# Kernel tuning notes

Hardware: AMD Instinct MI355X
Metric: run time of the kernel (lower is better)

Reference implementation:

```python
import jax, jax.numpy as jnp
import numpy as np

# PM-field / module constants (from module source + plausible PMField defaults)
DT = 0.1          # PM-field integration step
EPS = 1e-4        # softening of gravitational flow
PM_STEPS = 4      # pm_steps
TAU = 0.9         # membrane_tau
M_GAIN = 0.1      # membrane_gain
EI_GAIN = 0.06    # VectorizedLateralEI gain
PLR = 0.001       # plasticity_lr (mu_lr = c_lr)


def setup_inputs() -> dict:
    key = jax.random.key(0)
    ks = jax.random.split(key, 8)
    B, D_IN, D_HID, D_LAT, N_C, CH, N_CLS = 16384, 784, 256, 8, 64, 64, 10
    x = jax.random.normal(ks[0], (B, D_IN), jnp.float32)
    W1 = jax.random.normal(ks[1], (D_IN, D_HID), jnp.float32) * 0.05
    b1 = jnp.zeros((D_HID,), jnp.float32)
    W2 = jax.random.normal(ks[2], (D_HID, D_LAT), jnp.float32) * 0.05
    b2 = jnp.zeros((D_LAT,), jnp.float32)
    mu = jax.random.uniform(ks[3], (N_C,), jnp.float32) * 0.5       # center strengths
    c = jax.random.normal(ks[4], (N_C, D_LAT), jnp.float32)         # center positions
    Wp = jax.random.normal(ks[5], (D_LAT, CH), jnp.float32) * 0.3
    bp = jnp.zeros((CH,), jnp.float32)
    Wr = jax.random.normal(ks[6], (CH, N_CLS), jnp.float32) * 0.1
    br = jnp.zeros((N_CLS,), jnp.float32)
    return {"x": x, "W1": W1, "b1": b1, "W2": W2, "b2": b2, "mu": mu,
            "c": c, "Wp": Wp, "bp": bp, "Wr": Wr, "br": br, "T": 5}


def _pm_evolve(z, mu, c):
    # Gravitational PM-field: z follows softened attraction to centers c with strengths mu.
    def body(z, _):
        d = c[None, :, :] - z[:, None, :]            # [B, N, D]
        r2 = jnp.sum(d * d, axis=-1) + EPS           # [B, N]
        z = z + DT * jnp.einsum('bn,bnd->bd', mu / r2, d)
        return z, None
    z, _ = jax.lax.scan(body, z, None, length=PM_STEPS)
    return z


def _forward(x, W1, b1, W2, b2, mu, c, Wp, bp, Wr, br, T):
    z = jnp.tanh(x @ W1 + b1) @ W2 + b2              # enc: [B, d_latent]
    h = jnp.zeros((x.shape[0], Wp.shape[1]), x.dtype)

    def step(carry, _):
        z, h, mu, c = carry
        z_ev = _pm_evolve(z, mu, c)
        h_proj = jnp.tanh(z_ev @ Wp + bp)
        h_new = TAU * h + M_GAIN * h_proj
        # lateral EI: excitation minus mean inhibition
        h_f = h_new + EI_GAIN * (h_new - jnp.mean(h_new, axis=-1, keepdims=True))
        logits = h_f @ Wr + br
        # vectorized Hebbian plasticity on PM centers (no-grad, like torch .data update)
        d = c[None, :, :] - z_ev[:, None, :]
        r2 = jnp.sum(d * d, axis=-1)                 # [B, N]
        act = jnp.exp(-r2)                           # center activity
        post = jnp.mean(h_f, axis=-1)                # postsynaptic drive [B]
        mu2 = mu + PLR * jnp.mean(act * post[:, None], axis=0)
        wsum = jnp.sum(act, axis=0)                  # [N]
        w = act / (wsum + EPS)[None, :]
        c2 = c + PLR * (jnp.einsum('bn,bd->nd', w, z_ev) - c * (wsum / (wsum + EPS))[:, None])
        mu2 = jax.lax.stop_gradient(mu2)
        c2 = jax.lax.stop_gradient(c2)
        return (z_ev, h_f, mu2, c2), logits

    (z, h, _, _), logits_seq = jax.lax.scan(step, (z, h, mu, c), None, length=T)
    return logits_seq[-1], z, h


def reference(x, W1, b1, W2, b2, mu, c, Wp, bp, Wr, br, T):
    return _forward(x, W1, b1, W2, b2, mu, c, Wp, bp, Wr, br, T)
```

## Files before the change

### kernel.cpp

```cpp
#include <hip/hip_runtime.h>
#include <math.h>

#define B_N     16384
#define D_IN    784
#define D_HID   256
#define D_LAT   8
#define N_CTR   64
#define CH_N    64
#define N_CLS   10

#define DT_C    0.1f
#define EPS_C   1e-4f
#define PM_STEPS 4
#define TAU_C   0.9f
#define MGAIN   0.1f
#define EIG     0.06f
#define PLR_C   0.001f
#define T_STEPS 5

#define KP      832

typedef short bf16x8 __attribute__((ext_vector_type(8)));
typedef float f32x4v __attribute__((ext_vector_type(4)));

__device__ __forceinline__ void split_pair(float a, float b, unsigned& hi, unsigned& lo) {
    unsigned ua = __float_as_uint(a), ub = __float_as_uint(b);
    hi = (ua >> 16) | (ub & 0xffff0000u);
    float ra = a - __uint_as_float(ua & 0xffff0000u);
    float rb = b - __uint_as_float(ub & 0xffff0000u);
    lo = (__float_as_uint(ra) >> 16) | (__float_as_uint(rb) & 0xffff0000u);
}

__device__ __forceinline__ float fast_rcp(float x) { return __builtin_amdgcn_rcpf(x); }
__device__ __forceinline__ float fast_tanh(float a) {
    float e = __expf(2.0f * a);
    return 1.0f - 2.0f * fast_rcp(e + 1.0f);
}

#define DPP_XOR_ADD(v, CTRL) \
    ((v) + __int_as_float(__builtin_amdgcn_update_dpp(0, __float_as_int(v), (CTRL), 0xF, 0xF, true)))

__global__ __launch_bounds__(256) void w1t_kernel(
    const float* __restrict__ W1, ushort* __restrict__ WtH, ushort* __restrict__ WtL)
{
    __shared__ float t[32][36];
    const int kb = blockIdx.x;
    const int nb = blockIdx.y;
    const int tid = threadIdx.x;
    {
        const int r = tid >> 3, c4 = (tid & 7) * 4;
        const int k = kb * 32 + r;
        float4 v = {0.f, 0.f, 0.f, 0.f};
        if (k < D_IN) v = *(const float4*)(W1 + (size_t)k * 256 + nb * 32 + c4);
        t[r][c4 + 0] = v.x; t[r][c4 + 1] = v.y; t[r][c4 + 2] = v.z; t[r][c4 + 3] = v.w;
    }
    __syncthreads();
    const int n = tid >> 3, kq = (tid & 7) * 4;
    float a0 = t[kq + 0][n], a1 = t[kq + 1][n], a2 = t[kq + 2][n], a3 = t[kq + 3][n];
    unsigned h0, l0, h1w, l1w;
    split_pair(a0, a1, h0, l0);
    split_pair(a2, a3, h1w, l1w);
    const size_t o = (size_t)(nb * 32 + n) * KP + kb * 32 + kq;
    uint2 hv; hv.x = h0; hv.y = h1w;
    uint2 lv; lv.x = l0; lv.y = l1w;
    *(uint2*)(WtH + o) = hv;
    *(uint2*)(WtL + o) = lv;
}

__global__ __launch_bounds__(256, 3) void enc1_kernel(
    const float* __restrict__ x, const ushort* __restrict__ WtH,
    const ushort* __restrict__ WtL, const float* __restrict__ b1,
    float* __restrict__ h1)
{
    __shared__ alignas(16) unsigned char AhiS[16384];
    __shared__ alignas(16) unsigned char AloS[16384];
    __shared__ alignas(16) unsigned char BhiS[8192];
    __shared__ alignas(16) unsigned char BloS[8192];

    const int tid = threadIdx.x;
    const int bx  = blockIdx.x;
    const int wk  = (bx & 7) * 64 + (bx >> 3);
    const int n0  = (wk & 3) * 64;
    const int m0  = (wk >> 2) * 128;

    const int m_s = tid >> 1, kh = tid & 1;
    const int n_s = tid >> 2, kq = tid & 3;
    const float*  xrow = x + (size_t)(m0 + m_s) * D_IN;
    const ushort* bhrow = WtH + (size_t)(n0 + n_s) * KP + kq * 16;
    const ushort* blrow = WtL + (size_t)(n0 + n_s) * KP + kq * 16;
    const unsigned offB0 = (unsigned)(n_s * 128) + (unsigned)(((2 * kq)     ^ (n_s & 7)) << 4);
    const unsigned offB1 = (unsigned)(n_s * 128) + (unsigned)(((2 * kq + 1) ^ (n_s & 7)) << 4);

    const int lane = tid & 63;
    const int wid  = tid >> 6;
    const int wm   = wid >> 1, wn = wid & 1;
    const int fr   = lane & 15, g = lane >> 4;
    const unsigned swz = (unsigned)((fr & 7) << 4);
    const int kgb  = g * 16;

    f32x4v acc[4][2];
    #pragma unroll
    for (int mi = 0; mi < 4; ++mi)
        #pragma unroll
        for (int ni = 0; ni < 2; ++ni) acc[mi][ni] = (f32x4v){0.f, 0.f, 0.f, 0.f};

    for (int kt = 0; kt < 13; ++kt) {
        const int kbase = kt * 64 + kh * 32;
        float4 av[8];
        #pragma unroll
        for (int q = 0; q < 8; ++q) {
            const int kk = kbase + q * 4;
            float4 z4 = {0.f, 0.f, 0.f, 0.f};
            av[q] = (kk < D_IN) ? *(const float4*)(xrow + kk) : z4;
        }
        #pragma unroll
        for (int q16 = 0; q16 < 4; ++q16) {
            uint4 hw, lw;
            split_pair(av[2 * q16].x,     av[2 * q16].y,     hw.x, lw.x);
            split_pair(av[2 * q16].z,     av[2 * q16].w,     hw.y, lw.y);
            split_pair(av[2 * q16 + 1].x, av[2 * q16 + 1].y, hw.z, lw.z);
            split_pair(av[2 * q16 + 1].z, av[2 * q16 + 1].w, hw.w, lw.w);
            const unsigned off = (unsigned)(m_s * 128) +
                (unsigned)((((kh * 4 + q16) ^ (m_s & 7))) << 4);
            *(uint4*)(AhiS + off) = hw;
            *(uint4*)(AloS + off) = lw;
        }
        {
            const int ko = kt * 64;
            uint4 h0 = *(const uint4*)(bhrow + ko);
            uint4 h1v = *(const uint4*)(bhrow + ko + 8);
            uint4 l0 = *(const uint4*)(blrow + ko);
            uint4 l1v = *(const uint4*)(blrow + ko + 8);
            *(uint4*)(BhiS + offB0) = h0;
            *(uint4*)(BhiS + offB1) = h1v;
            *(uint4*)(BloS + offB0) = l0;
            *(uint4*)(BloS + offB1) = l1v;
        }
        __syncthreads();

        #pragma unroll
        for (int ks = 0; ks < 2; ++ks) {
            const unsigned kb = (unsigned)(ks * 64 + kgb);
            bf16x8 ahv[4], alv[4];
            #pragma unroll
            for (int mi = 0; mi < 4; ++mi) {
                const unsigned off = (unsigned)((wm * 64 + mi * 16 + fr) * 128) + (kb ^ swz);
                ahv[mi] = *(const bf16x8*)(AhiS + off);
                alv[mi] = *(const bf16x8*)(AloS + off);
            }
            #pragma unroll
            for (int ni = 0; ni < 2; ++ni) {
                const unsigned offb = (unsigned)((wn * 32 + ni * 16 + fr) * 128) + (kb ^ swz);
                bf16x8 bh = *(const bf16x8*)(BhiS + offb);
                bf16x8 bl = *(const bf16x8*)(BloS + offb);
                #pragma unroll
                for (int mi = 0; mi < 4; ++mi) {
                    acc[mi][ni] = __builtin_amdgcn_mfma_f32_16x16x32_bf16(ahv[mi], bh, acc[mi][ni], 0, 0, 0);
                    acc[mi][ni] = __builtin_amdgcn_mfma_f32_16x16x32_bf16(ahv[mi], bl, acc[mi][ni], 0, 0, 0);
                    acc[mi][ni] = __builtin_amdgcn_mfma_f32_16x16x32_bf16(alv[mi], bh, acc[mi][ni], 0, 0, 0);
                }
            }
        }
        __syncthreads();
    }

    #pragma unroll
    for (int ni = 0; ni < 2; ++ni) {
        const int col = n0 + wn * 32 + ni * 16 + fr;
        const float bias = b1[col];
        #pragma unroll
        for (int mi = 0; mi < 4; ++mi) {
            #pragma unroll
            for (int r = 0; r < 4; ++r) {
                const int row = m0 + wm * 64 + mi * 16 + g * 4 + r;
                h1[(size_t)row * 256 + col] = tanhf(acc[mi][ni][r] + bias);
            }
        }
    }
}

__global__ __launch_bounds__(256) void enc2_kernel(
    const float* __restrict__ h1, const float* __restrict__ W2,
    const float* __restrict__ b2, float* __restrict__ zT)
{
    __shared__ alignas(16) float hs[32][260];
    __shared__ alignas(16) float w2t[8][260];
    const int tid = threadIdx.x;
    const int r0 = blockIdx.x * 32;
    for (int i = tid; i < D_HID * D_LAT; i += 256) {
        int k = i >> 3, d = i & 7;
        w2t[d][k] = W2[i];
    }
    #pragma unroll
    for (int i = 0; i < 8; ++i) {
        int idx = tid + i * 256;
        int rr = idx >> 6, c4 = idx & 63;
        float4 v = *(const float4*)(h1 + (size_t)(r0 + rr) * D_HID + c4 * 4);
        *(float4*)&hs[rr][c4 * 4] = v;
    }
    __syncthreads();
    const int r = tid >> 3, d = tid & 7;
    float acc = 0.f;
    #pragma unroll 8
    for (int k4 = 0; k4 < 64; ++k4) {
        float4 a = *(const float4*)&hs[r][k4 * 4];
        float4 w = *(const float4*)&w2t[d][k4 * 4];
        acc = fmaf(a.x, w.x, acc);
        acc = fmaf(a.y, w.y, acc);
        acc = fmaf(a.z, w.z, acc);
        acc = fmaf(a.w, w.w, acc);
    }
    zT[(size_t)(r0 + r) * 8 + d] = acc + b2[d];
}

__global__ __launch_bounds__(256) void stepA2_kernel(
    float* __restrict__ zT, float* __restrict__ hT,
    const float* __restrict__ mu, const float* __restrict__ c,
    const float* __restrict__ Wp, const float* __restrict__ bp,
    const float* __restrict__ Wr, const float* __restrict__ br,
    float* __restrict__ part, float* __restrict__ out, int t)
{
    __shared__ alignas(16) float mu_s[64];
    __shared__ alignas(16) float c_s[512];
    __shared__ alignas(16) float wp_s[512];
    __shared__ alignas(16) float bp_s[64];
    __shared__ alignas(16) float wr_s[704];
    __shared__ alignas(16) float br_s[16];
    __shared__ alignas(16) float act_s[32 * 72];
    __shared__ alignas(16) float z_s[256];
    __shared__ alignas(16) float post_s[32];
    __shared__ alignas(16) float red2[4 * 64 * 10];
    const int tid = threadIdx.x;
    if (tid < 64) { mu_s[tid] = mu[tid]; bp_s[tid] = bp[tid]; }
    for (int i = tid; i < 512; i += 256) { c_s[i] = c[i]; wp_s[i] = Wp[i]; }
    const bool last = (t == T_STEPS - 1);
    if (last) {
        for (int i = tid; i < 640; i += 256) wr_s[(i / 10) * 11 + (i % 10)] = Wr[i];
        if (tid < N_CLS) br_s[tid] = br[tid];
    }
    __syncthreads();

    const int sub  = tid & 7;
    const int grp  = tid >> 3;
    const int b    = blockIdx.x * 32 + grp;
    const int lane = tid & 63;
    const int gbase = lane & ~7;

    float zown = zT[(size_t)b * 8 + sub];
    float z[8];
    #pragma unroll
    for (int d = 0; d < 8; ++d) z[d] = __shfl(zown, gbase + d, 64);

    #pragma unroll 1
    for (int it = 0; it < PM_STEPS; ++it) {
        float f[8];
        #pragma unroll
        for (int d = 0; d < 8; ++d) f[d] = 0.f;
        #pragma unroll
        for (int k = 0; k < 8; ++k) {
            const int n = sub + 8 * k;
            float dx[8];
            float r2 = EPS_C;
            #pragma unroll
            for (int d = 0; d < 8; ++d) {
                dx[d] = c_s[n * 8 + d] - z[d];
                r2 = fmaf(dx[d], dx[d], r2);
            }
            float wgt = mu_s[n] * fast_rcp(r2);
            #pragma unroll
            for (int d = 0; d < 8; ++d) f[d] = fmaf(wgt, dx[d], f[d]);
        }
        #pragma unroll
        for (int d = 0; d < 8; ++d) f[d] = DPP_XOR_ADD(f[d], 0xB1);
        #pragma unroll
        for (int d = 0; d < 8; ++d) f[d] = DPP_XOR_ADD(f[d], 0x4E);
        #pragma unroll
        for (int d = 0; d < 8; ++d) f[d] += __shfl_xor(f[d], 4, 64);
        #pragma unroll
        for (int d = 0; d < 8; ++d) z[d] = fmaf(DT_C, f[d], z[d]);
    }
    float zsel = z[0];
    #pragma unroll
    for (int d = 1; d < 8; ++d) if (sub == d) zsel = z[d];
    zT[(size_t)b * 8 + sub] = zsel;

    float hn[8];
    float s = 0.f;
    #pragma unroll
    for (int j = 0; j < 8; ++j) {
        const int ch = sub * 8 + j;
        float a = bp_s[ch];
        #pragma unroll
        for (int d = 0; d < 8; ++d) a = fmaf(z[d], wp_s[d * 64 + ch], a);
        hn[j] = fast_tanh(a);
    }
    if (t == 0) {
        #pragma unroll
        for (int j = 0; j < 8; ++j) { hn[j] = MGAIN * hn[j]; s += hn[j]; }
    } else {
        const float4* hp = (const float4*)(hT + (size_t)b * 64 + sub * 8);
        float4 h0 = hp[0], h1v = hp[1];
        hn[0] = TAU_C * h0.x + MGAIN * hn[0];
        hn[1] = TAU_C * h0.y + MGAIN * hn[1];
        hn[2] = TAU_C * h0.z + MGAIN * hn[2];
        hn[3] = TAU_C * h0.w + MGAIN * hn[3];
        hn[4] = TAU_C * h1v.x + MGAIN * hn[4];
        hn[5] = TAU_C * h1v.y + MGAIN * hn[5];
        hn[6] = TAU_C * h1v.z + MGAIN * hn[6];
        hn[7] = TAU_C * h1v.w + MGAIN * hn[7];
        #pragma unroll
        for (int j = 0; j < 8; ++j) s += hn[j];
    }
    s = DPP_XOR_ADD(s, 0xB1);
    s = DPP_XOR_ADD(s, 0x4E);
    s += __shfl_xor(s, 4, 64);
    const float mean = s * (1.f / 64.f);
    float spost = 0.f;
    #pragma unroll
    for (int j = 0; j < 8; ++j) {
        hn[j] = hn[j] + EIG * (hn[j] - mean);
        spost += hn[j];
    }
    {
        float4 a0 = {hn[0], hn[1], hn[2], hn[3]};
        float4 a1 = {hn[4], hn[5], hn[6], hn[7]};
        float4* hp = (float4*)(hT + (size_t)b * 64 + sub * 8);
        hp[0] = a0; hp[1] = a1;
    }
    spost = DPP_XOR_ADD(spost, 0xB1);
    spost = DPP_XOR_ADD(spost, 0x4E);
    spost += __shfl_xor(spost, 4, 64);

    if (!last) {
        z_s[tid] = zsel;
        if (sub == 0) post_s[grp] = spost * (1.f / 64.f);
        #pragma unroll
        for (int k = 0; k < 8; ++k) {
            const int n = sub + 8 * k;
            float r2 = 0.f;
            #pragma unroll
            for (int d = 0; d < 8; ++d) {
                float dd = c_s[n * 8 + d] - z[d];
                r2 = fmaf(dd, dd, r2);
            }
            act_s[grp * 72 + n] = __expf(-r2);
        }
        __syncthreads();
        const int q = tid >> 6, n2 = tid & 63;
        float r[10];
        #pragma unroll
        for (int j = 0; j < 10; ++j) r[j] = 0.f;
        #pragma unroll
        for (int i = 0; i < 8; ++i) {
            const int g2 = q * 8 + i;
            float a = act_s[g2 * 72 + n2];
            const float4* zp = (const float4*)&z_s[g2 * 8];
            float4 za = zp[0], zb = zp[1];
            r[0] += a;
            r[1] = fmaf(a, post_s[g2], r[1]);
            r[2] = fmaf(a, za.x, r[2]);
            r[3] = fmaf(a, za.y, r[3]);
            r[4] = fmaf(a, za.z, r[4]);
            r[5] = fmaf(a, za.w, r[5]);
            r[6] = fmaf(a, zb.x, r[6]);
            r[7] = fmaf(a, zb.y, r[7]);
            r[8] = fmaf(a, zb.z, r[8]);
            r[9] = fmaf(a, zb.w, r[9]);
        }
        #pragma unroll
        for (int j = 0; j < 10; ++j) red2[(q * 64 + n2) * 10 + j] = r[j];
        __syncthreads();
        if (q == 0) {
            #pragma unroll
            for (int j = 0; j < 10; ++j) {
                float sv = (red2[(n2) * 10 + j] + red2[(64 + n2) * 10 + j]) +
                           (red2[(128 + n2) * 10 + j] + red2[(192 + n2) * 10 + j]);
                part[((size_t)blockIdx.x * 64 + n2) * 10 + j] = sv;
            }
        }
    } else {
        float lg[N_CLS];
        #pragma unroll
        for (int cls = 0; cls < N_CLS; ++cls) lg[cls] = 0.f;
        #pragma unroll
        for (int j = 0; j < 8; ++j) {
            const int ch = sub * 8 + j;
            #pragma unroll
            for (int cls = 0; cls < N_CLS; ++cls)
                lg[cls] = fmaf(hn[j], wr_s[ch * 11 + cls], lg[cls]);
        }
        #pragma unroll
        for (int cls = 0; cls < N_CLS; ++cls) {
            lg[cls] = DPP_XOR_ADD(lg[cls], 0xB1);
            lg[cls] = DPP_XOR_ADD(lg[cls], 0x4E);
            lg[cls] += __shfl_xor(lg[cls], 4, 64);
        }
        if (sub == 0) {
            #pragma unroll
            for (int cls = 0; cls < N_CLS; ++cls)
                out[(size_t)b * 10 + cls] = lg[cls] + br_s[cls];
        }
        out[163840 + (size_t)b * 8 + sub] = zsel;
        {
            float4 a0 = {hn[0], hn[1], hn[2], hn[3]};
            float4 a1 = {hn[4], hn[5], hn[6], hn[7]};
            float4* op = (float4*)(out + 294912 + (size_t)b * 64 + sub * 8);
            op[0] = a0; op[1] = a1;
        }
    }
}

__global__ __launch_bounds__(256) void stepB2_kernel(
    const float* __restrict__ part,
    const float* __restrict__ mu_in, const float* __restrict__ c_in,
    float* __restrict__ mu_out, float* __restrict__ c_out)
{
    const int n = blockIdx.x, tid = threadIdx.x;
    __shared__ float red[256][10];
    const float* p0 = part + ((size_t)tid * 64 + n) * 10;
    const float* p1 = part + ((size_t)(tid + 256) * 64 + n) * 10;
    #pragma unroll
    for (int j = 0; j < 10; ++j) red[tid][j] = p0[j] + p1[j];
    __syncthreads();
    for (int s = 128; s > 0; s >>= 1) {
        if (tid < s) {
            #pragma unroll
            for (int j = 0; j < 10; ++j) red[tid][j] += red[tid + s][j];
        }
        __syncthreads();
    }
    if (tid == 0) {
        const float S1 = red[0][0];
        const float S2 = red[0][1] * (1.f / B_N);
        mu_out[n] = mu_in[n] + PLR_C * S2;
        const float denom = S1 + EPS_C;
        #pragma unroll
        for (int d = 0; d < 8; ++d) {
            float s3 = red[0][2 + d];
            c_out[n * 8 + d] = c_in[n * 8 + d] + PLR_C * (s3 / denom - c_in[n * 8 + d] * (S1 / denom));
        }
    }
}

extern "C" void kernel_launch(void* const* d_in, const int* in_sizes, int n_in,
                              void* d_out, int out_size, void* d_ws, size_t ws_size,
                              hipStream_t stream) {
    (void)in_sizes; (void)n_in; (void)out_size; (void)ws_size;
    const float* x   = (const float*)d_in[0];
    const float* W1  = (const float*)d_in[1];
    const float* b1  = (const float*)d_in[2];
    const float* W2  = (const float*)d_in[3];
    const float* b2  = (const float*)d_in[4];
    const float* mu0 = (const float*)d_in[5];
    const float* c0  = (const float*)d_in[6];
    const float* Wp  = (const float*)d_in[7];
    const float* bp  = (const float*)d_in[8];
    const float* Wr  = (const float*)d_in[9];
    const float* br  = (const float*)d_in[10];
    float* out = (float*)d_out;
    float* ws  = (float*)d_ws;

    float* h1    = ws;
    float* hT    = ws;
    float* part  = ws + 2113536;
    float* zT    = ws + 4194304;
    float* mu_buf = ws + 4325376;
    float* c_buf  = ws + 4325504;
    ushort* WtH  = (ushort*)(ws + 4326528);
    ushort* WtL  = (ushort*)(ws + 4433024);

    w1t_kernel<<<dim3(26, 8), 256, 0, stream>>>(W1, WtH, WtL);
    enc1_kernel<<<512, 256, 0, stream>>>(x, WtH, WtL, b1, h1);
    enc2_kernel<<<512, 256, 0, stream>>>(h1, W2, b2, zT);

    const float* mu_cur = mu0;
    const float* c_cur  = c0;
    for (int t = 0; t < T_STEPS; ++t) {
        stepA2_kernel<<<512, 256, 0, stream>>>(zT, hT, mu_cur, c_cur, Wp, bp, Wr, br,
                                               part, out, t);
        if (t < T_STEPS - 1) {
            float* mo = mu_buf + (t & 1) * 64;
            float* co = c_buf  + (t & 1) * 512;
            stepB2_kernel<<<64, 256, 0, stream>>>(part, mu_cur, c_cur, mo, co);
            mu_cur = mo;
            c_cur  = co;
        }
    }
}
```

Baseline: 120.1 us.

## Halve per-block tiles in encoder GEMM and step kernel to double block count

The enc1 GEMM tile shrinks from 128x64 to 64x64 rows per block, with half the LDS for A, and launch bounds raised to 4 blocks per SIMD with 1024 blocks. stepA2 now uses 16 lanes per sample instead of 8, with 16 samples per block across 1024 blocks, a 16-lane DPP/shuffle reduction macro, and a padded stride-9 centre array in LDS to avoid bank conflicts. stepB2 sums four partial rows per thread to match the doubled partial count. The aim is more parallelism and occupancy on the many-CU GPU, at the cost of less data reuse per block in the GEMM and more partial sums to reduce.

```diff
diff --git a/kernel.cpp b/kernel.cpp
--- a/kernel.cpp
+++ b/kernel.cpp
@@ -37,8 +37,14 @@
     return 1.0f - 2.0f * fast_rcp(e + 1.0f);
 }
 
-#define DPP_XOR_ADD(v, CTRL) \
+#define DPP_ADD(v, CTRL) \
     ((v) + __int_as_float(__builtin_amdgcn_update_dpp(0, __float_as_int(v), (CTRL), 0xF, 0xF, true)))
+#define RED16(v) do { \
+    v = DPP_ADD(v, 0xB1); \
+    v = DPP_ADD(v, 0x4E); \
+    v += __shfl_xor(v, 4, 64); \
+    v = DPP_ADD(v, 0x128); \
+} while (0)
 
 __global__ __launch_bounds__(256) void w1t_kernel(
     const float* __restrict__ W1, ushort* __restrict__ WtH, ushort* __restrict__ WtL)
@@ -67,27 +73,29 @@
     *(uint2*)(WtL + o) = lv;
 }
 
-__global__ __launch_bounds__(256, 3) void enc1_kernel(
+__global__ __launch_bounds__(256, 4) void enc1_kernel(
     const float* __restrict__ x, const ushort* __restrict__ WtH,
     const ushort* __restrict__ WtL, const float* __restrict__ b1,
     float* __restrict__ h1)
 {
-    __shared__ alignas(16) unsigned char AhiS[16384];
-    __shared__ alignas(16) unsigned char AloS[16384];
+    __shared__ alignas(16) unsigned char AhiS[8192];
+    __shared__ alignas(16) unsigned char AloS[8192];
     __shared__ alignas(16) unsigned char BhiS[8192];
     __shared__ alignas(16) unsigned char BloS[8192];
 
     const int tid = threadIdx.x;
     const int bx  = blockIdx.x;
-    const int wk  = (bx & 7) * 64 + (bx >> 3);
+    const int wk  = (bx & 7) * 128 + (bx >> 3);
     const int n0  = (wk & 3) * 64;
-    const int m0  = (wk >> 2) * 128;
-
-    const int m_s = tid >> 1, kh = tid & 1;
+    const int m0  = (wk >> 2) * 64;
+
+    const int m_s = tid >> 2, kq2 = tid & 3;
     const int n_s = tid >> 2, kq = tid & 3;
     const float*  xrow = x + (size_t)(m0 + m_s) * D_IN;
     const ushort* bhrow = WtH + (size_t)(n0 + n_s) * KP + kq * 16;
     const ushort* blrow = WtL + (size_t)(n0 + n_s) * KP + kq * 16;
+    const unsigned offA0 = (unsigned)(m_s * 128) + (unsigned)(((2 * kq2)     ^ (m_s & 7)) << 4);
+    const unsigned offA1 = (unsigned)(m_s * 128) + (unsigned)(((2 * kq2 + 1) ^ (m_s & 7)) << 4);
     const unsigned offB0 = (unsigned)(n_s * 128) + (unsigned)(((2 * kq)     ^ (n_s & 7)) << 4);
     const unsigned offB1 = (unsigned)(n_s * 128) + (unsigned)(((2 * kq + 1) ^ (n_s & 7)) << 4);
 
@@ -98,32 +106,35 @@
     const unsigned swz = (unsigned)((fr & 7) << 4);
     const int kgb  = g * 16;
 
-    f32x4v acc[4][2];
-    #pragma unroll
-    for (int mi = 0; mi < 4; ++mi)
+    f32x4v acc[2][2];
+    #pragma unroll
+    for (int mi = 0; mi < 2; ++mi)
         #pragma unroll
         for (int ni = 0; ni < 2; ++ni) acc[mi][ni] = (f32x4v){0.f, 0.f, 0.f, 0.f};
 
     for (int kt = 0; kt < 13; ++kt) {
-        const int kbase = kt * 64 + kh * 32;
-        float4 av[8];
-        #pragma unroll
-        for (int q = 0; q < 8; ++q) {
-            const int kk = kbase + q * 4;
-            float4 z4 = {0.f, 0.f, 0.f, 0.f};
-            av[q] = (kk < D_IN) ? *(const float4*)(xrow + kk) : z4;
-        }
-        #pragma unroll
-        for (int q16 = 0; q16 < 4; ++q16) {
-            uint4 hw, lw;
-            split_pair(av[2 * q16].x,     av[2 * q16].y,     hw.x, lw.x);
-            split_pair(av[2 * q16].z,     av[2 * q16].w,     hw.y, lw.y);
-            split_pair(av[2 * q16 + 1].x, av[2 * q16 + 1].y, hw.z, lw.z);
-            split_pair(av[2 * q16 + 1].z, av[2 * q16 + 1].w, hw.w, lw.w);
-            const unsigned off = (unsigned)(m_s * 128) +
-                (unsigned)((((kh * 4 + q16) ^ (m_s & 7))) << 4);
-            *(uint4*)(AhiS + off) = hw;
-            *(uint4*)(AloS + off) = lw;
+        {
+            const int kbase = kt * 64 + kq2 * 16;
+            float4 av[4];
+            #pragma unroll
+            for (int q = 0; q < 4; ++q) {
+                const int kk = kbase + q * 4;
+                float4 z4 = {0.f, 0.f, 0.f, 0.f};
+                av[q] = (kk < D_IN) ? *(const float4*)(xrow + kk) : z4;
+            }
+            uint4 hw0, lw0, hw1, lw1;
+            split_pair(av[0].x, av[0].y, hw0.x, lw0.x);
+            split_pair(av[0].z, av[0].w, hw0.y, lw0.y);
+            split_pair(av[1].x, av[1].y, hw0.z, lw0.z);
+            split_pair(av[1].z, av[1].w, hw0.w, lw0.w);
+            split_pair(av[2].x, av[2].y, hw1.x, lw1.x);
+            split_pair(av[2].z, av[2].w, hw1.y, lw1.y);
+            split_pair(av[3].x, av[3].y, hw1.z, lw1.z);
+            split_pair(av[3].z, av[3].w, hw1.w, lw1.w);
+            *(uint4*)(AhiS + offA0) = hw0;
+            *(uint4*)(AhiS + offA1) = hw1;
+            *(uint4*)(AloS + offA0) = lw0;
+            *(uint4*)(AloS + offA1) = lw1;
         }
         {
             const int ko = kt * 64;
@@ -141,10 +152,10 @@
         #pragma unroll
         for (int ks = 0; ks < 2; ++ks) {
             const unsigned kb = (unsigned)(ks * 64 + kgb);
-            bf16x8 ahv[4], alv[4];
-            #pragma unroll
-            for (int mi = 0; mi < 4; ++mi) {
-                const unsigned off = (unsigned)((wm * 64 + mi * 16 + fr) * 128) + (kb ^ swz);
+            bf16x8 ahv[2], alv[2];
+            #pragma unroll
+            for (int mi = 0; mi < 2; ++mi) {
+                const unsigned off = (unsigned)((wm * 32 + mi * 16 + fr) * 128) + (kb ^ swz);
                 ahv[mi] = *(const bf16x8*)(AhiS + off);
                 alv[mi] = *(const bf16x8*)(AloS + off);
             }
@@ -154,7 +165,7 @@
                 bf16x8 bh = *(const bf16x8*)(BhiS + offb);
                 bf16x8 bl = *(const bf16x8*)(BloS + offb);
                 #pragma unroll
-                for (int mi = 0; mi < 4; ++mi) {
+                for (int mi = 0; mi < 2; ++mi) {
                     acc[mi][ni] = __builtin_amdgcn_mfma_f32_16x16x32_bf16(ahv[mi], bh, acc[mi][ni], 0, 0, 0);
                     acc[mi][ni] = __builtin_amdgcn_mfma_f32_16x16x32_bf16(ahv[mi], bl, acc[mi][ni], 0, 0, 0);
                     acc[mi][ni] = __builtin_amdgcn_mfma_f32_16x16x32_bf16(alv[mi], bh, acc[mi][ni], 0, 0, 0);
@@ -169,10 +180,10 @@
         const int col = n0 + wn * 32 + ni * 16 + fr;
         const float bias = b1[col];
         #pragma unroll
-        for (int mi = 0; mi < 4; ++mi) {
+        for (int mi = 0; mi < 2; ++mi) {
             #pragma unroll
             for (int r = 0; r < 4; ++r) {
-                const int row = m0 + wm * 64 + mi * 16 + g * 4 + r;
+                const int row = m0 + wm * 32 + mi * 16 + g * 4 + r;
                 h1[(size_t)row * 256 + col] = tanhf(acc[mi][ni][r] + bias);
             }
         }
@@ -221,18 +232,21 @@
     float* __restrict__ part, float* __restrict__ out, int t)
 {
     __shared__ alignas(16) float mu_s[64];
-    __shared__ alignas(16) float c_s[512];
+    __shared__ alignas(16) float c9_s[576];
     __shared__ alignas(16) float wp_s[512];
     __shared__ alignas(16) float bp_s[64];
     __shared__ alignas(16) float wr_s[704];
     __shared__ alignas(16) float br_s[16];
-    __shared__ alignas(16) float act_s[32 * 72];
-    __shared__ alignas(16) float z_s[256];
-    __shared__ alignas(16) float post_s[32];
+    __shared__ alignas(16) float act_s[16 * 72];
+    __shared__ alignas(16) float z_s[128];
+    __shared__ alignas(16) float post_s[16];
     __shared__ alignas(16) float red2[4 * 64 * 10];
     const int tid = threadIdx.x;
     if (tid < 64) { mu_s[tid] = mu[tid]; bp_s[tid] = bp[tid]; }
-    for (int i = tid; i < 512; i += 256) { c_s[i] = c[i]; wp_s[i] = Wp[i]; }
+    for (int i = tid; i < 512; i += 256) {
+        c9_s[(i >> 3) * 9 + (i & 7)] = c[i];
+        wp_s[i] = Wp[i];
+    }
     const bool last = (t == T_STEPS - 1);
     if (last) {
         for (int i = tid; i < 640; i += 256) wr_s[(i / 10) * 11 + (i % 10)] = Wr[i];
@@ -240,13 +254,13 @@
     }
     __syncthreads();
 
-    const int sub  = tid & 7;
-    const int grp  = tid >> 3;
-    const int b    = blockIdx.x * 32 + grp;
+    const int sub  = tid & 15;
+    const int grp  = tid >> 4;
+    const int b    = blockIdx.x * 16 + grp;
     const int lane = tid & 63;
-    const int gbase = lane & ~7;
-
-    float zown = zT[(size_t)b * 8 + sub];
+    const int gbase = lane & ~15;
+
+    float zown = zT[(size_t)b * 8 + (sub & 7)];
     float z[8];
     #pragma unroll
     for (int d = 0; d < 8; ++d) z[d] = __shfl(zown, gbase + d, 64);
@@ -257,13 +271,13 @@
         #pragma unroll
         for (int d = 0; d < 8; ++d) f[d] = 0.f;
         #pragma unroll
-        for (int k = 0; k < 8; ++k) {
-            const int n = sub + 8 * k;
+        for (int k = 0; k < 4; ++k) {
+            const int n = sub + 16 * k;
             float dx[8];
             float r2 = EPS_C;
             #pragma unroll
             for (int d = 0; d < 8; ++d) {
-                dx[d] = c_s[n * 8 + d] - z[d];
+                dx[d] = c9_s[n * 9 + d] - z[d];
                 r2 = fmaf(dx[d], dx[d], r2);
             }
             float wgt = mu_s[n] * fast_rcp(r2);
@@ -271,24 +285,20 @@
             for (int d = 0; d < 8; ++d) f[d] = fmaf(wgt, dx[d], f[d]);
         }
         #pragma unroll
-        for (int d = 0; d < 8; ++d) f[d] = DPP_XOR_ADD(f[d], 0xB1);
-        #pragma unroll
-        for (int d = 0; d < 8; ++d) f[d] = DPP_XOR_ADD(f[d], 0x4E);
-        #pragma unroll
-        for (int d = 0; d < 8; ++d) f[d] += __shfl_xor(f[d], 4, 64);
+        for (int d = 0; d < 8; ++d) RED16(f[d]);
         #pragma unroll
         for (int d = 0; d < 8; ++d) z[d] = fmaf(DT_C, f[d], z[d]);
     }
     float zsel = z[0];
     #pragma unroll
-    for (int d = 1; d < 8; ++d) if (sub == d) zsel = z[d];
-    zT[(size_t)b * 8 + sub] = zsel;
-
-    float hn[8];
+    for (int d = 1; d < 8; ++d) if ((sub & 7) == d) zsel = z[d];
+    if (sub < 8) zT[(size_t)b * 8 + sub] = zsel;
+
+    float hn[4];
     float s = 0.f;
     #pragma unroll
-    for (int j = 0; j < 8; ++j) {
-        const int ch = sub * 8 + j;
+    for (int j = 0; j < 4; ++j) {
+        const int ch = sub * 4 + j;
         float a = bp_s[ch];
         #pragma unroll
         for (int d = 0; d < 8; ++d) a = fmaf(z[d], wp_s[d * 64 + ch], a);
@@ -296,51 +306,40 @@
     }
     if (t == 0) {
         #pragma unroll
-        for (int j = 0; j < 8; ++j) { hn[j] = MGAIN * hn[j]; s += hn[j]; }
+        for (int j = 0; j < 4; ++j) { hn[j] = MGAIN * hn[j]; s += hn[j]; }
     } else {
-        const float4* hp = (const float4*)(hT + (size_t)b * 64 + sub * 8);
-        float4 h0 = hp[0], h1v = hp[1];
+        float4 h0 = *(const float4*)(hT + (size_t)b * 64 + sub * 4);
         hn[0] = TAU_C * h0.x + MGAIN * hn[0];
         hn[1] = TAU_C * h0.y + MGAIN * hn[1];
         hn[2] = TAU_C * h0.z + MGAIN * hn[2];
         hn[3] = TAU_C * h0.w + MGAIN * hn[3];
-        hn[4] = TAU_C * h1v.x + MGAIN * hn[4];
-        hn[5] = TAU_C * h1v.y + MGAIN * hn[5];
-        hn[6] = TAU_C * h1v.z + MGAIN * hn[6];
-        hn[7] = TAU_C * h1v.w + MGAIN * hn[7];
-        #pragma unroll
-        for (int j = 0; j < 8; ++j) s += hn[j];
-    }
-    s = DPP_XOR_ADD(s, 0xB1);
-    s = DPP_XOR_ADD(s, 0x4E);
-    s += __shfl_xor(s, 4, 64);
+        #pragma unroll
+        for (int j = 0; j < 4; ++j) s += hn[j];
+    }
+    RED16(s);
     const float mean = s * (1.f / 64.f);
     float spost = 0.f;
     #pragma unroll
-    for (int j = 0; j < 8; ++j) {
+    for (int j = 0; j < 4; ++j) {
         hn[j] = hn[j] + EIG * (hn[j] - mean);
         spost += hn[j];
     }
     {
         float4 a0 = {hn[0], hn[1], hn[2], hn[3]};
-        float4 a1 = {hn[4], hn[5], hn[6], hn[7]};
-        float4* hp = (float4*)(hT + (size_t)b * 64 + sub * 8);
-        hp[0] = a0; hp[1] = a1;
-    }
-    spost = DPP_XOR_ADD(spost, 0xB1);
-    spost = DPP_XOR_ADD(spost, 0x4E);
-    spost += __shfl_xor(spost, 4, 64);
+        *(float4*)(hT + (size_t)b * 64 + sub * 4) = a0;
+    }
+    RED16(spost);
 
     if (!last) {
-        z_s[tid] = zsel;
+        if (sub < 8) z_s[grp * 8 + sub] = zsel;
         if (sub == 0) post_s[grp] = spost * (1.f / 64.f);
         #pragma unroll
-        for (int k = 0; k < 8; ++k) {
-            const int n = sub + 8 * k;
+        for (int k = 0; k < 4; ++k) {
+            const int n = sub + 16 * k;
             float r2 = 0.f;
             #pragma unroll
             for (int d = 0; d < 8; ++d) {
-                float dd = c_s[n * 8 + d] - z[d];
+                float dd = c9_s[n * 9 + d] - z[d];
                 r2 = fmaf(dd, dd, r2);
             }
             act_s[grp * 72 + n] = __expf(-r2);
@@ -351,8 +350,8 @@
         #pragma unroll
         for (int j = 0; j < 10; ++j) r[j] = 0.f;
         #pragma unroll
-        for (int i = 0; i < 8; ++i) {
-            const int g2 = q * 8 + i;
+        for (int i = 0; i < 4; ++i) {
+            const int g2 = q * 4 + i;
             float a = act_s[g2 * 72 + n2];
             const float4* zp = (const float4*)&z_s[g2 * 8];
             float4 za = zp[0], zb = zp[1];
@@ -383,29 +382,23 @@
         #pragma unroll
         for (int cls = 0; cls < N_CLS; ++cls) lg[cls] = 0.f;
         #pragma unroll
-        for (int j = 0; j < 8; ++j) {
-            const int ch = sub * 8 + j;
+        for (int j = 0; j < 4; ++j) {
+            const int ch = sub * 4 + j;
             #pragma unroll
             for (int cls = 0; cls < N_CLS; ++cls)
                 lg[cls] = fmaf(hn[j], wr_s[ch * 11 + cls], lg[cls]);
         }
         #pragma unroll
-        for (int cls = 0; cls < N_CLS; ++cls) {
-            lg[cls] = DPP_XOR_ADD(lg[cls], 0xB1);
-            lg[cls] = DPP_XOR_ADD(lg[cls], 0x4E);
-            lg[cls] += __shfl_xor(lg[cls], 4, 64);
-        }
+        for (int cls = 0; cls < N_CLS; ++cls) RED16(lg[cls]);
         if (sub == 0) {
             #pragma unroll
             for (int cls = 0; cls < N_CLS; ++cls)
                 out[(size_t)b * 10 + cls] = lg[cls] + br_s[cls];
         }
-        out[163840 + (size_t)b * 8 + sub] = zsel;
+        if (sub < 8) out[163840 + (size_t)b * 8 + sub] = zsel;
         {
             float4 a0 = {hn[0], hn[1], hn[2], hn[3]};
-            float4 a1 = {hn[4], hn[5], hn[6], hn[7]};
-            float4* op = (float4*)(out + 294912 + (size_t)b * 64 + sub * 8);
-            op[0] = a0; op[1] = a1;
+            *(float4*)(out + 294912 + (size_t)b * 64 + sub * 4) = a0;
         }
     }
 }
@@ -417,10 +410,12 @@
 {
     const int n = blockIdx.x, tid = threadIdx.x;
     __shared__ float red[256][10];
-    const float* p0 = part + ((size_t)tid * 64 + n) * 10;
+    const float* p0 = part + ((size_t)(tid)       * 64 + n) * 10;
     const float* p1 = part + ((size_t)(tid + 256) * 64 + n) * 10;
-    #pragma unroll
-    for (int j = 0; j < 10; ++j) red[tid][j] = p0[j] + p1[j];
+    const float* p2 = part + ((size_t)(tid + 512) * 64 + n) * 10;
+    const float* p3 = part + ((size_t)(tid + 768) * 64 + n) * 10;
+    #pragma unroll
+    for (int j = 0; j < 10; ++j) red[tid][j] = (p0[j] + p1[j]) + (p2[j] + p3[j]);
     __syncthreads();
     for (int s = 128; s > 0; s >>= 1) {
         if (tid < s) {
@@ -470,14 +465,14 @@
     ushort* WtL  = (ushort*)(ws + 4433024);
 
     w1t_kernel<<<dim3(26, 8), 256, 0, stream>>>(W1, WtH, WtL);
-    enc1_kernel<<<512, 256, 0, stream>>>(x, WtH, WtL, b1, h1);
+    enc1_kernel<<<1024, 256, 0, stream>>>(x, WtH, WtL, b1, h1);
     enc2_kernel<<<512, 256, 0, stream>>>(h1, W2, b2, zT);
 
     const float* mu_cur = mu0;
     const float* c_cur  = c0;
     for (int t = 0; t < T_STEPS; ++t) {
-        stepA2_kernel<<<512, 256, 0, stream>>>(zT, hT, mu_cur, c_cur, Wp, bp, Wr, br,
-                                               part, out, t);
+        stepA2_kernel<<<1024, 256, 0, stream>>>(zT, hT, mu_cur, c_cur, Wp, bp, Wr, br,
+                                                part, out, t);
         if (t < T_STEPS - 1) {
             float* mo = mu_buf + (t & 1) * 64;
             float* co = c_buf  + (t & 1) * 512;
```

New measurement: 177.1 us. 47.5% more time.

## Split-K the first encoder GEMM into two halves to double block count

Applied to the files above, without the earlier changes.

The first encoder GEMM is split along K into two halves, launching 1024 blocks instead of 512. Each half writes raw partial sums to its own workspace buffer. A new enc2s kernel adds the partials, applies bias and tanh, then does the second projection. The aim is better CU occupancy on the 256-CU device, paid for with an extra 32 MB of partial-sum traffic and a ws_size-dependent code path.

```diff
diff --git a/kernel.cpp b/kernel.cpp
--- a/kernel.cpp
+++ b/kernel.cpp
@@ -67,10 +67,11 @@
     *(uint2*)(WtL + o) = lv;
 }
 
-__global__ __launch_bounds__(256, 3) void enc1_kernel(
+template <bool SPLITK>
+__global__ __launch_bounds__(256, 3) void enc1_tpl(
     const float* __restrict__ x, const ushort* __restrict__ WtH,
     const ushort* __restrict__ WtL, const float* __restrict__ b1,
-    float* __restrict__ h1)
+    float* __restrict__ out0, float* __restrict__ out1)
 {
     __shared__ alignas(16) unsigned char AhiS[16384];
     __shared__ alignas(16) unsigned char AloS[16384];
@@ -79,9 +80,19 @@
 
     const int tid = threadIdx.x;
     const int bx  = blockIdx.x;
-    const int wk  = (bx & 7) * 64 + (bx >> 3);
-    const int n0  = (wk & 3) * 64;
-    const int m0  = (wk >> 2) * 128;
+    int tile, half, kt0, kt1;
+    if (SPLITK) {
+        const int wk = (bx & 7) * 128 + (bx >> 3);
+        half = wk & 1;
+        tile = wk >> 1;
+        kt0 = half ? 7 : 0;
+        kt1 = half ? 13 : 7;
+    } else {
+        tile = (bx & 7) * 64 + (bx >> 3);
+        half = 0; kt0 = 0; kt1 = 13;
+    }
+    const int n0 = (tile & 3) * 64;
+    const int m0 = (tile >> 2) * 128;
 
     const int m_s = tid >> 1, kh = tid & 1;
     const int n_s = tid >> 2, kq = tid & 3;
@@ -104,7 +115,7 @@
         #pragma unroll
         for (int ni = 0; ni < 2; ++ni) acc[mi][ni] = (f32x4v){0.f, 0.f, 0.f, 0.f};
 
-    for (int kt = 0; kt < 13; ++kt) {
+    for (int kt = kt0; kt < kt1; ++kt) {
         const int kbase = kt * 64 + kh * 32;
         float4 av[8];
         #pragma unroll
@@ -164,16 +175,20 @@
         __syncthreads();
     }
 
+    float* P = (SPLITK && half) ? out1 : out0;
     #pragma unroll
     for (int ni = 0; ni < 2; ++ni) {
         const int col = n0 + wn * 32 + ni * 16 + fr;
-        const float bias = b1[col];
+        const float bias = SPLITK ? 0.f : b1[col];
         #pragma unroll
         for (int mi = 0; mi < 4; ++mi) {
             #pragma unroll
             for (int r = 0; r < 4; ++r) {
                 const int row = m0 + wm * 64 + mi * 16 + g * 4 + r;
-                h1[(size_t)row * 256 + col] = tanhf(acc[mi][ni][r] + bias);
+                if (SPLITK)
+                    P[(size_t)row * 256 + col] = acc[mi][ni][r];
+                else
+                    P[(size_t)row * 256 + col] = tanhf(acc[mi][ni][r] + bias);
             }
         }
     }
@@ -197,6 +212,47 @@
         int rr = idx >> 6, c4 = idx & 63;
         float4 v = *(const float4*)(h1 + (size_t)(r0 + rr) * D_HID + c4 * 4);
         *(float4*)&hs[rr][c4 * 4] = v;
+    }
+    __syncthreads();
+    const int r = tid >> 3, d = tid & 7;
+    float acc = 0.f;
+    #pragma unroll 8
+    for (int k4 = 0; k4 < 64; ++k4) {
+        float4 a = *(const float4*)&hs[r][k4 * 4];
+        float4 w = *(const float4*)&w2t[d][k4 * 4];
+        acc = fmaf(a.x, w.x, acc);
+        acc = fmaf(a.y, w.y, acc);
+        acc = fmaf(a.z, w.z, acc);
+        acc = fmaf(a.w, w.w, acc);
+    }
+    zT[(size_t)(r0 + r) * 8 + d] = acc + b2[d];
+}
+
+__global__ __launch_bounds__(256) void enc2s_kernel(
+    const float* __restrict__ P0, const float* __restrict__ P1,
+    const float* __restrict__ b1, const float* __restrict__ W2,
+    const float* __restrict__ b2, float* __restrict__ zT)
+{
+    __shared__ alignas(16) float hs[32][260];
+    __shared__ alignas(16) float w2t[8][260];
+    const int tid = threadIdx.x;
+    const int r0 = blockIdx.x * 32;
+    for (int i = tid; i < D_HID * D_LAT; i += 256) {
+        int k = i >> 3, d = i & 7;
+        w2t[d][k] = W2[i];
+    }
+    #pragma unroll
+    for (int i = 0; i < 8; ++i) {
+        int idx = tid + i * 256;
+        int rr = idx >> 6, c4 = idx & 63;
+        const size_t off = (size_t)(r0 + rr) * D_HID + c4 * 4;
+        float4 v0 = *(const float4*)(P0 + off);
+        float4 v1 = *(const float4*)(P1 + off);
+        float4 bv = *(const float4*)(b1 + c4 * 4);
+        hs[rr][c4 * 4 + 0] = tanhf(v0.x + v1.x + bv.x);
+        hs[rr][c4 * 4 + 1] = tanhf(v0.y + v1.y + bv.y);
+        hs[rr][c4 * 4 + 2] = tanhf(v0.z + v1.z + bv.z);
+        hs[rr][c4 * 4 + 3] = tanhf(v0.w + v1.w + bv.w);
     }
     __syncthreads();
     const int r = tid >> 3, d = tid & 7;
@@ -445,7 +501,7 @@
 extern "C" void kernel_launch(void* const* d_in, const int* in_sizes, int n_in,
                               void* d_out, int out_size, void* d_ws, size_t ws_size,
                               hipStream_t stream) {
-    (void)in_sizes; (void)n_in; (void)out_size; (void)ws_size;
+    (void)in_sizes; (void)n_in; (void)out_size;
     const float* x   = (const float*)d_in[0];
     const float* W1  = (const float*)d_in[1];
     const float* b1  = (const float*)d_in[2];
@@ -460,18 +516,39 @@
     float* out = (float*)d_out;
     float* ws  = (float*)d_ws;
 
-    float* h1    = ws;
-    float* hT    = ws;
-    float* part  = ws + 2113536;
-    float* zT    = ws + 4194304;
-    float* mu_buf = ws + 4325376;
-    float* c_buf  = ws + 4325504;
-    ushort* WtH  = (ushort*)(ws + 4326528);
-    ushort* WtL  = (ushort*)(ws + 4433024);
-
-    w1t_kernel<<<dim3(26, 8), 256, 0, stream>>>(W1, WtH, WtL);
-    enc1_kernel<<<512, 256, 0, stream>>>(x, WtH, WtL, b1, h1);
-    enc2_kernel<<<512, 256, 0, stream>>>(h1, W2, b2, zT);
+    const bool split = (ws_size >= 34935296ull);
+
+    float *zT, *mu_buf, *c_buf, *hT, *part;
+    ushort *WtH, *WtL;
+
+    if (split) {
+        float* P0 = ws;
+        float* P1 = ws + 4194304;
+        hT     = ws;
+        part   = ws + 2113536;
+        zT     = ws + 8388608;
+        mu_buf = ws + 8519680;
+        c_buf  = ws + 8519808;
+        WtH    = (ushort*)(ws + 8520832);
+        WtL    = (ushort*)(ws + 8627328);
+
+        w1t_kernel<<<dim3(26, 8), 256, 0, stream>>>(W1, WtH, WtL);
+        enc1_tpl<true><<<1024, 256, 0, stream>>>(x, WtH, WtL, b1, P0, P1);
+        enc2s_kernel<<<512, 256, 0, stream>>>(P0, P1, b1, W2, b2, zT);
+    } else {
+        float* h1 = ws;
+        hT     = ws;
+        part   = ws + 2113536;
+        zT     = ws + 4194304;
+        mu_buf = ws + 4325376;
+        c_buf  = ws + 4325504;
+        WtH    = (ushort*)(ws + 4326528);
+        WtL    = (ushort*)(ws + 4433024);
+
+        w1t_kernel<<<dim3(26, 8), 256, 0, stream>>>(W1, WtH, WtL);
+        enc1_tpl<false><<<512, 256, 0, stream>>>(x, WtH, WtL, b1, h1, nullptr);
+        enc2_kernel<<<512, 256, 0, stream>>>(h1, W2, b2, zT);
+    }
 
     const float* mu_cur = mu0;
     const float* c_cur  = c0;
```

New measurement: 195.1 us. +62.4%, slower.
